# Optimization experiments

Measured on AMD Instinct MI355X. Metric: run time of the kernel, lower is better.

Reference implementation:

```python
import jax, jax.numpy as jnp
import numpy as np

N_NODES = 100000
N_EDGES = 3200000
N_GRAPHS = 512
F_IN = 35
F_OUT = 128


def setup_inputs() -> dict:
    key = jax.random.key(0)
    ks = jax.random.split(key, 16)
    x = jax.random.normal(ks[0], (N_NODES, F_IN), dtype=jnp.float32)
    edge_index = jax.random.randint(ks[1], (2, N_EDGES), 0, N_NODES, dtype=jnp.int32)
    batch = jnp.sort(jax.random.randint(ks[2], (N_NODES,), 0, N_GRAPHS, dtype=jnp.int32))
    def lin(k, fin, fout):
        s = 1.0 / np.sqrt(fin)
        return jax.random.uniform(k, (fin, fout), jnp.float32, -s, s)
    return {
        "x": x, "edge_index": edge_index, "batch": batch,
        # SAGEConv 1 (35 -> 35): lin_l acts on aggregated neighbors (has bias), lin_r on root (no bias)
        "Wl1": lin(ks[3], F_IN, F_IN), "bl1": jnp.zeros((F_IN,), jnp.float32), "Wr1": lin(ks[4], F_IN, F_IN),
        # SAGEConv 2 (35 -> 128)
        "Wl2": lin(ks[5], F_IN, F_OUT), "bl2": jnp.zeros((F_OUT,), jnp.float32), "Wr2": lin(ks[6], F_IN, F_OUT),
        # FC head
        "Wg1": lin(ks[7], F_OUT, F_OUT), "bg1": jnp.zeros((F_OUT,), jnp.float32),
        "Wg2": lin(ks[8], F_OUT, F_OUT), "bg2": jnp.zeros((F_OUT,), jnp.float32),
        "Wo": lin(ks[9], F_OUT, 1), "bo": jnp.zeros((1,), jnp.float32),
    }


def _sage_conv(x, src, dst, Wl, bl, Wr):
    # mean aggregation over incoming edges (src -> dst), PyG SAGEConv default
    msg = x[src]                                               # [E, F] gather
    s = jax.ops.segment_sum(msg, dst, num_segments=N_NODES)    # [N, F]
    cnt = jax.ops.segment_sum(jnp.ones((src.shape[0],), x.dtype), dst, num_segments=N_NODES)
    agg = s / jnp.maximum(cnt, 1.0)[:, None]
    return agg @ Wl + bl + x @ Wr


def reference(x, edge_index, batch, Wl1, bl1, Wr1, Wl2, bl2, Wr2, Wg1, bg1, Wg2, bg2, Wo, bo):
    src, dst = edge_index[0], edge_index[1]
    h = _sage_conv(x, src, dst, Wl1, bl1, Wr1)   # [N, 35]
    h = jax.nn.relu(h)
    h = _sage_conv(h, src, dst, Wl2, bl2, Wr2)   # [N, 128]
    # global max pool over each graph in the batch
    g = jax.ops.segment_max(h, batch, num_segments=N_GRAPHS)  # [G, 128]
    g = jax.nn.relu(g @ Wg1 + bg1)
    g = jax.nn.relu(g @ Wg2 + bg2)
    return g @ Wo + bo                            # [G, 1]
```

## Files before the change

kernel.cpp:

```cpp
#include <hip/hip_runtime.h>
#include <hip/hip_bf16.h>
#include <math.h>

#define FIN 35
#define FOUT 128
#define NGRAPHS 512
#define PWA 32
#define PWB 4
#define RP 36
#define STRIP1 64
#define STRIP2 32
#define CHUNK 8192
#define MAXBUCK 512
#define MAXBE 12288

typedef _Float16 half8 __attribute__((ext_vector_type(8)));
typedef _Float16 half4 __attribute__((ext_vector_type(4)));

__device__ __forceinline__ unsigned int enc_f32(float f) {
    unsigned int u = __float_as_uint(f);
    return (u & 0x80000000u) ? ~u : (u | 0x80000000u);
}
__device__ __forceinline__ float dec_f32(unsigned int u) {
    unsigned int b = (u & 0x80000000u) ? (u ^ 0x80000000u) : ~u;
    return __uint_as_float(b);
}


__global__ __launch_bounds__(256) void hist1_kernel(const int* __restrict__ dst,
                                                    int* __restrict__ counts,
                                                    int E, int nblk1, int nbuck) {
    __shared__ int h[MAXBUCK];
    for (int t = threadIdx.x; t < nbuck; t += 256) h[t] = 0;
    __syncthreads();
    int base = blockIdx.x * CHUNK;
    int end = min(base + CHUNK, E);
    for (int e = base + threadIdx.x; e < end; e += 256)
        atomicAdd(&h[dst[e] >> 8], 1);
    __syncthreads();
    for (int t = threadIdx.x; t < nbuck; t += 256)
        counts[t * nblk1 + blockIdx.x] = h[t];
}

__global__ void partial_reduce_kernel(const int* __restrict__ v_in, int* __restrict__ partial, int SC) {
    int i = blockIdx.x * 256 + threadIdx.x;
    int v = (i < SC) ? v_in[i] : 0;
    #pragma unroll
    for (int off = 32; off > 0; off >>= 1) v += __shfl_down(v, off, 64);
    __shared__ int w[4];
    if ((threadIdx.x & 63) == 0) w[threadIdx.x >> 6] = v;
    __syncthreads();
    if (threadIdx.x == 0) partial[blockIdx.x] = w[0] + w[1] + w[2] + w[3];
}

__global__ void scan_partials_kernel(int* __restrict__ partial, int NB) {
    __shared__ int lds[1024];
    int t = threadIdx.x;
    int v = (t < NB) ? partial[t] : 0;
    lds[t] = v;
    __syncthreads();
    for (int off = 1; off < 1024; off <<= 1) {
        int tv = (t >= off) ? lds[t - off] : 0;
        __syncthreads();
        lds[t] += tv;
        __syncthreads();
    }
    if (t < NB) partial[t] = lds[t] - v;
}

__global__ void scan_final_kernel(const int* __restrict__ v_in, const int* __restrict__ partial,
                                  int* __restrict__ outx, int SC) {
    __shared__ int lds[256];
    int i = blockIdx.x * 256 + threadIdx.x;
    int v = (i < SC) ? v_in[i] : 0;
    lds[threadIdx.x] = v;
    __syncthreads();
    for (int off = 1; off < 256; off <<= 1) {
        int tv = (threadIdx.x >= off) ? lds[threadIdx.x - off] : 0;
        __syncthreads();
        lds[threadIdx.x] += tv;
        __syncthreads();
    }
    int excl = lds[threadIdx.x] - v + partial[blockIdx.x];
    if (i < SC) {
        outx[i] = excl;
        if (i == SC - 1) outx[SC] = excl + v;
    }
}

__global__ __launch_bounds__(256) void scatter1_kernel(const int* __restrict__ src,
                                                       const int* __restrict__ dst,
                                                       const int* __restrict__ offs,
                                                       int* __restrict__ ebuf,
                                                       int E, int nblk1, int nbuck) {
    __shared__ int cur[MAXBUCK];
    for (int t = threadIdx.x; t < nbuck; t += 256) cur[t] = offs[t * nblk1 + blockIdx.x];
    __syncthreads();
    int base = blockIdx.x * CHUNK;
    int end = min(base + CHUNK, E);
    for (int e = base + threadIdx.x; e < end; e += 256) {
        int d = dst[e];
        int p = atomicAdd(&cur[d >> 8], 1);
        ebuf[p] = (src[e] << 8) | (d & 255);
    }
}

__global__ __launch_bounds__(256) void csr2_kernel(const int* __restrict__ ebuf,
                                                   const int* __restrict__ offs,
                                                   int* __restrict__ row_ptr,
                                                   int* __restrict__ hsplit,
                                                   int* __restrict__ esrc,
                                                   int E, int nblk1, int nbuck, int N, int halfN) {
    __shared__ int h[512];
    __shared__ int scn[256];
    __shared__ int cur[512];
    __shared__ int e_sh[MAXBE];
    int b = blockIdx.x;
    int t = threadIdx.x;
    int bstart = offs[b * nblk1];
    int bend = (b + 1 < nbuck) ? offs[(b + 1) * nblk1] : E;
    int cnt = bend - bstart;
    bool fit = (cnt <= MAXBE);

    if (fit)
        for (int k = t; k < cnt; k += 256) e_sh[k] = ebuf[bstart + k];
    h[t] = 0; h[t + 256] = 0;
    __syncthreads();
    for (int k = t; k < cnt; k += 256) {
        int e = fit ? e_sh[k] : ebuf[bstart + k];
        int bin = ((e & 255) << 1) | ((e >> 8) >= halfN ? 1 : 0);
        atomicAdd(&h[bin], 1);
    }
    __syncthreads();

    int v0 = h[2 * t];
    int v1 = h[2 * t + 1];
    int pair = v0 + v1;
    scn[t] = pair;
    __syncthreads();
    for (int off = 1; off < 256; off <<= 1) {
        int tv = (t >= off) ? scn[t - off] : 0;
        __syncthreads();
        scn[t] += tv;
        __syncthreads();
    }
    int base = bstart + scn[t] - pair;
    int node = (b << 8) + t;
    if (node < N) {
        row_ptr[node] = base;
        hsplit[node] = base + v0;
    }
    if (b == 0 && t == 0) row_ptr[N] = E;
    cur[2 * t] = base;
    cur[2 * t + 1] = base + v0;
    __syncthreads();

    for (int k = t; k < cnt; k += 256) {
        int e = fit ? e_sh[k] : ebuf[bstart + k];
        int bin = ((e & 255) << 1) | ((e >> 8) >= halfN ? 1 : 0);
        int p = atomicAdd(&cur[bin], 1);
        esrc[p] = e >> 8;
    }
}

__global__ void repack_kernel(const float* __restrict__ x,
                              _Float16* __restrict__ xA, _Float16* __restrict__ xB, int N) {
    int t = blockIdx.x * 256 + threadIdx.x;
    int NA = N * PWA;
    if (t < NA) {
        int n = t >> 5;
        int f = t & 31;
        xA[t] = (_Float16)x[(long long)n * FIN + f];
    } else if (t < NA + N * PWB) {
        int c = t - NA;
        int n = c >> 2;
        int f3 = c & 3;
        float v = (f3 < 3) ? x[(long long)n * FIN + 32 + f3] : 0.0f;
        xB[c] = (_Float16)v;
    }
}

__global__ __launch_bounds__(256) void gather3_kernel(const _Float16* __restrict__ pA,
                                                      const _Float16* __restrict__ pB,
                                                      const int* __restrict__ row_ptr,
                                                      const int* __restrict__ hsplit,
                                                      const int* __restrict__ esrc,
                                                      float* __restrict__ spA,
                                                      float* __restrict__ spB,
                                                      int N, int Wtot, int WS) {
    int q = blockIdx.x & 7;
    int m = blockIdx.x >> 3;
    int w = q * WS + m * 256 + threadIdx.x;
    int wend = min((q + 1) * WS, Wtot);
    if (w >= wend) return;
    int NI = N * 8;
    int pass = w / NI;
    int t = w - pass * NI;
    int n = t >> 3;

    if (pass < 2) {
        int quad = (t >> 1) & 3;
        int q2 = t & 1;
        int b = (pass == 0) ? row_ptr[n] : hsplit[n];
        int e = (pass == 0) ? hsplit[n] : row_ptr[n + 1];
        int len = e - b;
        int k0 = b + ((len * q2) >> 1);
        int k1 = b + ((len * (q2 + 1)) >> 1);
        const _Float16* base = pA + (quad << 3);

        float a0[8] = {0,0,0,0,0,0,0,0}, a1[8] = {0,0,0,0,0,0,0,0};
        float a2[8] = {0,0,0,0,0,0,0,0}, a3[8] = {0,0,0,0,0,0,0,0};
        int k = k0;
        for (; k + 4 <= k1; k += 4) {
            int s0 = esrc[k], s1 = esrc[k + 1], s2 = esrc[k + 2], s3 = esrc[k + 3];
            half8 v0 = *(const half8*)(base + ((long long)s0 << 5));
            half8 v1 = *(const half8*)(base + ((long long)s1 << 5));
            half8 v2 = *(const half8*)(base + ((long long)s2 << 5));
            half8 v3 = *(const half8*)(base + ((long long)s3 << 5));
            #pragma unroll
            for (int i = 0; i < 8; ++i) {
                a0[i] += (float)v0[i];
                a1[i] += (float)v1[i];
                a2[i] += (float)v2[i];
                a3[i] += (float)v3[i];
            }
        }
        for (; k < k1; ++k) {
            half8 v = *(const half8*)(base + ((long long)esrc[k] << 5));
            #pragma unroll
            for (int i = 0; i < 8; ++i) a0[i] += (float)v[i];
        }

        float s[8];
        #pragma unroll
        for (int i = 0; i < 8; ++i) {
            float p = (a0[i] + a1[i]) + (a2[i] + a3[i]);
            p += __shfl_xor(p, 1, 64);
            s[i] = p;
        }
        if (q2 == 0) {
            float* outp = spA + ((long long)pass * N + n) * PWA + (quad << 3);
            float4 r0, r1;
            r0.x = s[0]; r0.y = s[1]; r0.z = s[2]; r0.w = s[3];
            r1.x = s[4]; r1.y = s[5]; r1.z = s[6]; r1.w = s[7];
            *(float4*)outp = r0;
            *(float4*)(outp + 4) = r1;
        }
    } else {
        int q8 = t & 7;
        int b = row_ptr[n];
        int e = row_ptr[n + 1];
        int len = e - b;
        int k0 = b + ((len * q8) >> 3);
        int k1 = b + ((len * (q8 + 1)) >> 3);

        float a0[4] = {0,0,0,0}, a1[4] = {0,0,0,0};
        int k = k0;
        for (; k + 2 <= k1; k += 2) {
            int s0 = esrc[k], s1 = esrc[k + 1];
            half4 v0 = *(const half4*)(pB + ((long long)s0 << 2));
            half4 v1 = *(const half4*)(pB + ((long long)s1 << 2));
            #pragma unroll
            for (int i = 0; i < 4; ++i) {
                a0[i] += (float)v0[i];
                a1[i] += (float)v1[i];
            }
        }
        for (; k < k1; ++k) {
            half4 v = *(const half4*)(pB + ((long long)esrc[k] << 2));
            #pragma unroll
            for (int i = 0; i < 4; ++i) a0[i] += (float)v[i];
        }

        float s[4];
        #pragma unroll
        for (int i = 0; i < 4; ++i) {
            float p = a0[i] + a1[i];
            p += __shfl_xor(p, 1, 64);
            p += __shfl_xor(p, 2, 64);
            p += __shfl_xor(p, 4, 64);
            s[i] = p;
        }
        if (q8 == 0) {
            float4 r;
            r.x = s[0]; r.y = s[1]; r.z = s[2]; r.w = s[3];
            *(float4*)(spB + ((long long)n << 2)) = r;
        }
    }
}

__global__ __launch_bounds__(256) void nu1_kernel(const float* __restrict__ x,
                                                  const float* __restrict__ spA,
                                                  const float* __restrict__ spB,
                                                  const int* __restrict__ row_ptr,
                                                  const float* __restrict__ Wl,
                                                  const float* __restrict__ bl,
                                                  const float* __restrict__ Wr,
                                                  _Float16* __restrict__ h1A,
                                                  _Float16* __restrict__ h1B,
                                                  int N) {
    __shared__ float x_sh[STRIP1 * RP];
    __shared__ float s_sh[STRIP1 * RP];
    __shared__ int deg_sh[STRIP1];

    int node0 = blockIdx.x * STRIP1;
    if (node0 >= N) return;
    int nn = min(STRIP1, N - node0);
    int tot = nn * FIN;

    for (int t = threadIdx.x; t < STRIP1; t += 256) {
        x_sh[t * RP + 35] = 0.0f;
        s_sh[t * RP + 35] = 0.0f;
    }
    if (threadIdx.x < nn)
        deg_sh[threadIdx.x] = row_ptr[node0 + threadIdx.x + 1] - row_ptr[node0 + threadIdx.x];
    for (int t = threadIdx.x; t < tot; t += 256) {
        int nl = t / FIN;
        int i = t - nl * FIN;
        long long node = node0 + nl;
        x_sh[nl * RP + i] = x[node * FIN + i];
        float sv = (i < 32) ? (spA[node * PWA + i] + spA[((long long)N + node) * PWA + i])
                            : spB[(node << 2) + (i - 32)];
        s_sh[nl * RP + i] = sv;
    }
    __syncthreads();

    int wave = threadIdx.x >> 6;
    int j = threadIdx.x & 63;
    if (j >= FIN) return;

    float wl[36], wr[36];
    #pragma unroll
    for (int i = 0; i < FIN; ++i) {
        wl[i] = Wl[i * FIN + j];
        wr[i] = Wr[i * FIN + j];
    }
    wl[35] = 0.0f; wr[35] = 0.0f;
    float blj = bl[j];

    int nstart = wave * 16;
    int nend = min(nstart + 16, nn);
    for (int nl = nstart; nl < nend; ++nl) {
        float accS = 0.0f;
        float accX = blj;
        #pragma unroll
        for (int c = 0; c < 9; ++c) {
            float4 sv = *(const float4*)&s_sh[nl * RP + 4 * c];
            float4 xv = *(const float4*)&x_sh[nl * RP + 4 * c];
            accS = fmaf(sv.x, wl[4 * c],     accS);
            accS = fmaf(sv.y, wl[4 * c + 1], accS);
            accS = fmaf(sv.z, wl[4 * c + 2], accS);
            accS = fmaf(sv.w, wl[4 * c + 3], accS);
            accX = fmaf(xv.x, wr[4 * c],     accX);
            accX = fmaf(xv.y, wr[4 * c + 1], accX);
            accX = fmaf(xv.z, wr[4 * c + 2], accX);
            accX = fmaf(xv.w, wr[4 * c + 3], accX);
        }
        float inv = 1.0f / (float)max(deg_sh[nl], 1);
        float acc = fmaxf(fmaf(accS, inv, accX), 0.0f);
        long long node = node0 + nl;
        if (j < 32) {
            h1A[(node << 5) + j] = (_Float16)acc;
        } else {
            h1B[(node << 2) + (j - 32)] = (_Float16)acc;
            if (j == 34) h1B[(node << 2) + 3] = (_Float16)0.0f;
        }
    }
}

__global__ __launch_bounds__(128) void nu2_pool_kernel(const _Float16* __restrict__ h1A,
                                                       const _Float16* __restrict__ h1B,
                                                       const float* __restrict__ spA,
                                                       const float* __restrict__ spB,
                                                       const int* __restrict__ row_ptr,
                                                       const float* __restrict__ Wl,
                                                       const float* __restrict__ bl,
                                                       const float* __restrict__ Wr,
                                                       const int* __restrict__ batch,
                                                       unsigned int* __restrict__ genc,
                                                       int N) {
    __shared__ float s_sh[STRIP2 * RP];
    __shared__ float h_sh[STRIP2 * RP];
    __shared__ int b_sh[STRIP2];
    __shared__ int deg_sh[STRIP2];
    int node0 = blockIdx.x * STRIP2;
    if (node0 >= N) return;
    int nn = min(STRIP2, N - node0);
    int tot = nn * FIN;

    for (int t = threadIdx.x; t < STRIP2; t += 128) {
        s_sh[t * RP + 35] = 0.0f;
        h_sh[t * RP + 35] = 0.0f;
    }
    if (threadIdx.x < nn) {
        b_sh[threadIdx.x] = batch[node0 + threadIdx.x];
        deg_sh[threadIdx.x] = row_ptr[node0 + threadIdx.x + 1] - row_ptr[node0 + threadIdx.x];
    }
    for (int t = threadIdx.x; t < tot; t += 128) {
        int nl = t / FIN;
        int i = t - nl * FIN;
        long long node = node0 + nl;
        float hv = (i < 32) ? (float)h1A[(node << 5) + i]
                            : (float)h1B[(node << 2) + (i - 32)];
        h_sh[nl * RP + i] = hv;
        float sv = (i < 32) ? (spA[node * PWA + i] + spA[((long long)N + node) * PWA + i])
                            : spB[(node << 2) + (i - 32)];
        s_sh[nl * RP + i] = sv;
    }
    __syncthreads();

    int j = threadIdx.x;
    float wl[36], wr[36];
    #pragma unroll
    for (int i = 0; i < FIN; ++i) {
        wl[i] = Wl[i * FOUT + j];
        wr[i] = Wr[i * FOUT + j];
    }
    wl[35] = 0.0f; wr[35] = 0.0f;
    float blj = bl[j];

    int curg = b_sh[0];
    float m = -INFINITY;
    for (int nl = 0; nl < nn; ++nl) {
        float accS = 0.0f;
        float accH = blj;
        #pragma unroll
        for (int c = 0; c < 9; ++c) {
            float4 sv = *(const float4*)&s_sh[nl * RP + 4 * c];
            float4 hv = *(const float4*)&h_sh[nl * RP + 4 * c];
            accS = fmaf(sv.x, wl[4 * c],     accS);
            accS = fmaf(sv.y, wl[4 * c + 1], accS);
            accS = fmaf(sv.z, wl[4 * c + 2], accS);
            accS = fmaf(sv.w, wl[4 * c + 3], accS);
            accH = fmaf(hv.x, wr[4 * c],     accH);
            accH = fmaf(hv.y, wr[4 * c + 1], accH);
            accH = fmaf(hv.z, wr[4 * c + 2], accH);
            accH = fmaf(hv.w, wr[4 * c + 3], accH);
        }
        float inv = 1.0f / (float)max(deg_sh[nl], 1);
        float acc = fmaf(accS, inv, accH);
        int g = b_sh[nl];
        if (g != curg) {
            atomicMax(&genc[curg * FOUT + j], enc_f32(m));
            curg = g;
            m = acc;
        } else {
            m = fmaxf(m, acc);
        }
    }
    atomicMax(&genc[curg * FOUT + j], enc_f32(m));
}

__global__ void head_kernel(const unsigned int* __restrict__ genc,
                            const float* __restrict__ Wg1, const float* __restrict__ bg1,
                            const float* __restrict__ Wg2, const float* __restrict__ bg2,
                            const float* __restrict__ Wo,  const float* __restrict__ bo,
                            float* __restrict__ out) {
    __shared__ float a[FOUT];
    __shared__ float c[FOUT];
    __shared__ float red[2];
    int g = blockIdx.x;
    int j = threadIdx.x;

    a[j] = dec_f32(genc[g * FOUT + j]);
    __syncthreads();

    float acc = bg1[j];
    #pragma unroll 8
    for (int i = 0; i < FOUT; ++i) acc = fmaf(a[i], Wg1[i * FOUT + j], acc);
    c[j] = fmaxf(acc, 0.0f);
    __syncthreads();

    acc = bg2[j];
    #pragma unroll 8
    for (int i = 0; i < FOUT; ++i) acc = fmaf(c[i], Wg2[i * FOUT + j], acc);
    float t = fmaxf(acc, 0.0f) * Wo[j];

    #pragma unroll
    for (int off = 32; off > 0; off >>= 1) t += __shfl_down(t, off, 64);
    if ((threadIdx.x & 63) == 0) red[threadIdx.x >> 6] = t;
    __syncthreads();
    if (threadIdx.x == 0) out[g] = red[0] + red[1] + bo[0];
}

extern "C" void kernel_launch(void* const* d_in, const int* in_sizes, int n_in,
                              void* d_out, int out_size, void* d_ws, size_t ws_size,
                              hipStream_t stream) {
    const float* x    = (const float*)d_in[0];
    const int*   ei   = (const int*)  d_in[1];
    const int*   batch= (const int*)  d_in[2];
    const float* Wl1  = (const float*)d_in[3];
    const float* bl1  = (const float*)d_in[4];
    const float* Wr1  = (const float*)d_in[5];
    const float* Wl2  = (const float*)d_in[6];
    const float* bl2  = (const float*)d_in[7];
    const float* Wr2  = (const float*)d_in[8];
    const float* Wg1  = (const float*)d_in[9];
    const float* bg1  = (const float*)d_in[10];
    const float* Wg2  = (const float*)d_in[11];
    const float* bg2  = (const float*)d_in[12];
    const float* Wo   = (const float*)d_in[13];
    const float* bo   = (const float*)d_in[14];
    float* out = (float*)d_out;

    const int N = in_sizes[0] / FIN;
    const int E = in_sizes[1] / 2;
    const int* src = ei;
    const int* dst = ei + E;
    const int halfN = N >> 1;

    const int nblk1 = (E + CHUNK - 1) / CHUNK;
    const int nbuck = (N + 255) >> 8;
    const int SC = nbuck * nblk1;
    const int NB2 = (SC + 255) / 256;

    char* ws = (char*)d_ws;
    size_t off = 0;
    auto alloc = [&](size_t bytes) { char* p = ws + off; off += (bytes + 255) & ~255ull; return p; };
    int*          counts  = (int*)alloc((size_t)SC * 4);
    int*          offs    = (int*)alloc((size_t)(SC + 1) * 4);
    int*          partial = (int*)alloc(1024 * 4);
    int*          row_ptr = (int*)alloc((size_t)(N + 1) * 4);
    int*          hsplit  = (int*)alloc((size_t)N * 4);
    int*          esrc    = (int*)alloc((size_t)E * 4);
    char*         regionA = (char*)alloc((size_t)E * 4);
    _Float16*     xA      = (_Float16*)alloc((size_t)N * PWA * 2);
    _Float16*     xB      = (_Float16*)alloc((size_t)N * PWB * 2);
    float*        spA     = (float*)alloc((size_t)2 * N * PWA * 4);
    float*        spB     = (float*)alloc((size_t)N * PWB * 4);
    unsigned int* genc    = (unsigned int*)alloc((size_t)NGRAPHS * FOUT * 4);
    int*       ebuf = (int*)regionA;
    _Float16*  h1A  = (_Float16*)regionA;
    _Float16*  h1B  = (_Float16*)(regionA + (size_t)N * PWA * 2);
    (void)ws_size; (void)n_in; (void)out_size;

    const int BS = 256;
    const int Wtot = N * 24;
    int WS = ((Wtot / 8 + BS - 1) / BS) * BS;
    const int bpx = WS / BS;
    const int rpb = (N * 36 + BS - 1) / BS;
    int nu1b = (N + STRIP1 - 1) / STRIP1;
    int nu2b = (N + STRIP2 - 1) / STRIP2;

    hipLaunchKernelGGL(hist1_kernel, dim3(nblk1), dim3(BS), 0, stream, dst, counts, E, nblk1, nbuck);
    hipLaunchKernelGGL(partial_reduce_kernel, dim3(NB2), dim3(BS), 0, stream, counts, partial, SC);
    hipLaunchKernelGGL(scan_partials_kernel, dim3(1), dim3(1024), 0, stream, partial, NB2);
    hipLaunchKernelGGL(scan_final_kernel, dim3(NB2), dim3(BS), 0, stream, counts, partial, offs, SC);
    hipLaunchKernelGGL(scatter1_kernel, dim3(nblk1), dim3(BS), 0, stream, src, dst, offs, ebuf, E, nblk1, nbuck);
    hipLaunchKernelGGL(csr2_kernel, dim3(nbuck), dim3(BS), 0, stream,
                       ebuf, offs, row_ptr, hsplit, esrc, E, nblk1, nbuck, N, halfN);

    hipLaunchKernelGGL(repack_kernel, dim3(rpb), dim3(BS), 0, stream, x, xA, xB, N);
    hipLaunchKernelGGL(gather3_kernel, dim3(8 * bpx), dim3(BS), 0, stream,
                       xA, xB, row_ptr, hsplit, esrc, spA, spB, N, Wtot, WS);
    hipLaunchKernelGGL(nu1_kernel, dim3(nu1b), dim3(BS), 0, stream,
                       x, spA, spB, row_ptr, Wl1, bl1, Wr1, h1A, h1B, N);

    hipLaunchKernelGGL(gather3_kernel, dim3(8 * bpx), dim3(BS), 0, stream,
                       h1A, h1B, row_ptr, hsplit, esrc, spA, spB, N, Wtot, WS);
    hipMemsetAsync(genc, 0, (size_t)NGRAPHS * FOUT * 4, stream);
    hipLaunchKernelGGL(nu2_pool_kernel, dim3(nu2b), dim3(128), 0, stream,
                       h1A, h1B, spA, spB, row_ptr, Wl2, bl2, Wr2, batch, genc, N);

    hipLaunchKernelGGL(head_kernel, dim3(NGRAPHS), dim3(FOUT), 0, stream,
                       genc, Wg1, bg1, Wg2, bg2, Wo, bo, out);
}
```

Before: 371.2 us.

## Use MFMA fp16 matrix cores for second SAGE layer with split-weight precision

Replaces the scalar FMA per-node loop of the second SAGEConv plus max-pool with a 64-node-strip kernel that packs the mean-aggregated neighbours and root features into a swizzled fp16 LDS tile and multiplies them with a concatenated [Wl;Wr] matrix using 16x16x32 f16 MFMA. A small prep kernel splits the weights into high and low fp16 parts, so two MFMA passes recover near-fp32 weight precision, and writes them in fragment layout. The activations are rounded to fp16, which adds precision risk. The pooling then reads the results back from LDS and does atomicMax per graph run.

```diff
diff --git a/kernel.cpp b/kernel.cpp
--- a/kernel.cpp
+++ b/kernel.cpp
@@ -9,13 +9,17 @@
 #define PWB 4
 #define RP 36
 #define STRIP1 64
-#define STRIP2 32
 #define CHUNK 8192
 #define MAXBUCK 512
 #define MAXBE 12288
 
+#define STRIPM 64
+#define HROW 130
+#define NFRAG 48
+
 typedef _Float16 half8 __attribute__((ext_vector_type(8)));
 typedef _Float16 half4 __attribute__((ext_vector_type(4)));
+typedef float f32x4 __attribute__((ext_vector_type(4)));
 
 __device__ __forceinline__ unsigned int enc_f32(float f) {
     unsigned int u = __float_as_uint(f);
@@ -368,87 +372,207 @@
     }
 }
 
-__global__ __launch_bounds__(128) void nu2_pool_kernel(const _Float16* __restrict__ h1A,
-                                                       const _Float16* __restrict__ h1B,
-                                                       const float* __restrict__ spA,
-                                                       const float* __restrict__ spB,
-                                                       const int* __restrict__ row_ptr,
-                                                       const float* __restrict__ Wl,
-                                                       const float* __restrict__ bl,
-                                                       const float* __restrict__ Wr,
-                                                       const int* __restrict__ batch,
-                                                       unsigned int* __restrict__ genc,
-                                                       int N) {
-    __shared__ float s_sh[STRIP2 * RP];
-    __shared__ float h_sh[STRIP2 * RP];
-    __shared__ int b_sh[STRIP2];
-    __shared__ int deg_sh[STRIP2];
-    int node0 = blockIdx.x * STRIP2;
+__global__ void wprep2_kernel(const float* __restrict__ Wl, const float* __restrict__ Wr,
+                              _Float16* __restrict__ wfrag) {
+    int f = blockIdx.x;
+    int l = threadIdx.x;
+    int ps = f / 24;
+    int rem = f % 24;
+    int ks = rem >> 3;
+    int nt = rem & 7;
+    int n = nt * 16 + (l & 15);
+    int kb = ks * 32 + ((l >> 4) << 3);
+    half8 o;
+    #pragma unroll
+    for (int e = 0; e < 8; ++e) {
+        int k = kb + e;
+        float v = 0.0f;
+        if (k < 35) v = Wl[k * FOUT + n];
+        else if (k >= 36 && k < 71) v = Wr[(k - 36) * FOUT + n];
+        _Float16 hi = (_Float16)v;
+        o[e] = ps ? (_Float16)(v - (float)hi) : hi;
+    }
+    *(half8*)(wfrag + ((size_t)f * 64 + l) * 8) = o;
+}
+
+__global__ __launch_bounds__(256) void nu2_pool_mfma_kernel(const _Float16* __restrict__ h1A,
+                                                            const _Float16* __restrict__ h1B,
+                                                            const float* __restrict__ spA,
+                                                            const float* __restrict__ spB,
+                                                            const int* __restrict__ row_ptr,
+                                                            const _Float16* __restrict__ wfrag,
+                                                            const float* __restrict__ bl,
+                                                            const int* __restrict__ batch,
+                                                            unsigned int* __restrict__ genc,
+                                                            int N) {
+    __shared__ __align__(16) float h_sh[STRIPM * HROW];
+    __shared__ int b_sh[STRIPM];
+
+    int node0 = blockIdx.x * STRIPM;
     if (node0 >= N) return;
-    int nn = min(STRIP2, N - node0);
-    int tot = nn * FIN;
-
-    for (int t = threadIdx.x; t < STRIP2; t += 128) {
-        s_sh[t * RP + 35] = 0.0f;
-        h_sh[t * RP + 35] = 0.0f;
-    }
-    if (threadIdx.x < nn) {
-        b_sh[threadIdx.x] = batch[node0 + threadIdx.x];
-        deg_sh[threadIdx.x] = row_ptr[node0 + threadIdx.x + 1] - row_ptr[node0 + threadIdx.x];
-    }
-    for (int t = threadIdx.x; t < tot; t += 128) {
-        int nl = t / FIN;
-        int i = t - nl * FIN;
-        long long node = node0 + nl;
-        float hv = (i < 32) ? (float)h1A[(node << 5) + i]
-                            : (float)h1B[(node << 2) + (i - 32)];
-        h_sh[nl * RP + i] = hv;
-        float sv = (i < 32) ? (spA[node * PWA + i] + spA[((long long)N + node) * PWA + i])
-                            : spB[(node << 2) + (i - 32)];
-        s_sh[nl * RP + i] = sv;
-    }
-    __syncthreads();
-
-    int j = threadIdx.x;
-    float wl[36], wr[36];
+    int nn = min(STRIPM, N - node0);
+
+    char* Ab = (char*)h_sh;
+    const int t = threadIdx.x;
+    const int lane = t & 63;
+    const int wv = t >> 6;
+
+    {
+        const int r = lane;
+        const long long node = (long long)node0 + r;
+        const bool valid = (r < nn);
+        const int sw = r & 7;
+        char* rowp = Ab + r * 256;
+
+        if (wv == 0) {
+            int dg = 1;
+            if (valid) dg = row_ptr[node + 1] - row_ptr[node];
+            float inv = 1.0f / (float)max(dg, 1);
+            #pragma unroll
+            for (int u = 0; u < 3; ++u) {
+                half8 h = {0,0,0,0,0,0,0,0};
+                if (valid) {
+                    const float* p = spA + node * 32 + u * 8;
+                    const float* q = spA + ((long long)N + node) * 32 + u * 8;
+                    float4 p0 = *(const float4*)p;
+                    float4 p1 = *(const float4*)(p + 4);
+                    float4 q0 = *(const float4*)q;
+                    float4 q1 = *(const float4*)(q + 4);
+                    h[0] = (_Float16)((p0.x + q0.x) * inv);
+                    h[1] = (_Float16)((p0.y + q0.y) * inv);
+                    h[2] = (_Float16)((p0.z + q0.z) * inv);
+                    h[3] = (_Float16)((p0.w + q0.w) * inv);
+                    h[4] = (_Float16)((p1.x + q1.x) * inv);
+                    h[5] = (_Float16)((p1.y + q1.y) * inv);
+                    h[6] = (_Float16)((p1.z + q1.z) * inv);
+                    h[7] = (_Float16)((p1.w + q1.w) * inv);
+                }
+                *(half8*)(rowp + ((u ^ sw) << 4)) = h;
+            }
+        } else if (wv == 1) {
+            int dg = 1;
+            if (valid) dg = row_ptr[node + 1] - row_ptr[node];
+            float inv = 1.0f / (float)max(dg, 1);
+            half8 h3 = {0,0,0,0,0,0,0,0};
+            half8 h4 = {0,0,0,0,0,0,0,0};
+            half8 h5 = {0,0,0,0,0,0,0,0};
+            if (valid) {
+                const float* p = spA + node * 32 + 24;
+                const float* q = spA + ((long long)N + node) * 32 + 24;
+                float4 p0 = *(const float4*)p;
+                float4 p1 = *(const float4*)(p + 4);
+                float4 q0 = *(const float4*)q;
+                float4 q1 = *(const float4*)(q + 4);
+                h3[0] = (_Float16)((p0.x + q0.x) * inv);
+                h3[1] = (_Float16)((p0.y + q0.y) * inv);
+                h3[2] = (_Float16)((p0.z + q0.z) * inv);
+                h3[3] = (_Float16)((p0.w + q0.w) * inv);
+                h3[4] = (_Float16)((p1.x + q1.x) * inv);
+                h3[5] = (_Float16)((p1.y + q1.y) * inv);
+                h3[6] = (_Float16)((p1.z + q1.z) * inv);
+                h3[7] = (_Float16)((p1.w + q1.w) * inv);
+                float4 sb = *(const float4*)(spB + (node << 2));
+                half4 ha = *(const half4*)(h1A + (node << 5));
+                h4[0] = (_Float16)(sb.x * inv);
+                h4[1] = (_Float16)(sb.y * inv);
+                h4[2] = (_Float16)(sb.z * inv);
+                h4[3] = (_Float16)(sb.w * inv);
+                h4[4] = ha[0]; h4[5] = ha[1]; h4[6] = ha[2]; h4[7] = ha[3];
+                half4 hb0 = *(const half4*)(h1A + (node << 5) + 4);
+                half4 hb1 = *(const half4*)(h1A + (node << 5) + 8);
+                h5[0] = hb0[0]; h5[1] = hb0[1]; h5[2] = hb0[2]; h5[3] = hb0[3];
+                h5[4] = hb1[0]; h5[5] = hb1[1]; h5[6] = hb1[2]; h5[7] = hb1[3];
+            }
+            *(half8*)(rowp + ((3 ^ sw) << 4)) = h3;
+            *(half8*)(rowp + ((4 ^ sw) << 4)) = h4;
+            *(half8*)(rowp + ((5 ^ sw) << 4)) = h5;
+        } else if (wv == 2) {
+            half8 h6 = {0,0,0,0,0,0,0,0};
+            half8 h7 = {0,0,0,0,0,0,0,0};
+            half8 h8 = {0,0,0,0,0,0,0,0};
+            if (valid) {
+                half4 a0 = *(const half4*)(h1A + (node << 5) + 12);
+                half4 a1 = *(const half4*)(h1A + (node << 5) + 16);
+                half4 a2 = *(const half4*)(h1A + (node << 5) + 20);
+                half4 a3 = *(const half4*)(h1A + (node << 5) + 24);
+                half4 a4 = *(const half4*)(h1A + (node << 5) + 28);
+                half4 b4 = *(const half4*)(h1B + (node << 2));
+                h6[0] = a0[0]; h6[1] = a0[1]; h6[2] = a0[2]; h6[3] = a0[3];
+                h6[4] = a1[0]; h6[5] = a1[1]; h6[6] = a1[2]; h6[7] = a1[3];
+                h7[0] = a2[0]; h7[1] = a2[1]; h7[2] = a2[2]; h7[3] = a2[3];
+                h7[4] = a3[0]; h7[5] = a3[1]; h7[6] = a3[2]; h7[7] = a3[3];
+                h8[0] = a4[0]; h8[1] = a4[1]; h8[2] = a4[2]; h8[3] = a4[3];
+                h8[4] = b4[0]; h8[5] = b4[1]; h8[6] = b4[2]; h8[7] = b4[3];
+            }
+            *(half8*)(rowp + ((6 ^ sw) << 4)) = h6;
+            *(half8*)(rowp + ((7 ^ sw) << 4)) = h7;
+            *(half8*)(rowp + ((8 ^ sw) << 4)) = h8;
+        } else {
+            half8 z = {0,0,0,0,0,0,0,0};
+            *(half8*)(rowp + ((9  ^ sw) << 4)) = z;
+            *(half8*)(rowp + ((10 ^ sw) << 4)) = z;
+            *(half8*)(rowp + ((11 ^ sw) << 4)) = z;
+            if (lane < nn) b_sh[lane] = batch[node0 + lane];
+        }
+    }
+    __syncthreads();
+
+    f32x4 acc[8];
     #pragma unroll
-    for (int i = 0; i < FIN; ++i) {
-        wl[i] = Wl[i * FOUT + j];
-        wr[i] = Wr[i * FOUT + j];
-    }
-    wl[35] = 0.0f; wr[35] = 0.0f;
-    float blj = bl[j];
-
-    int curg = b_sh[0];
-    float m = -INFINITY;
-    for (int nl = 0; nl < nn; ++nl) {
-        float accS = 0.0f;
-        float accH = blj;
+    for (int nt = 0; nt < 8; ++nt) acc[nt] = (f32x4){0.0f, 0.0f, 0.0f, 0.0f};
+
+    const int m0 = wv << 4;
+    const int rr = m0 + (lane & 15);
+    const int rsw = lane & 7;
+    const int g = lane >> 4;
+    const char* arow = Ab + rr * 256;
+
+    #pragma unroll
+    for (int ps = 0; ps < 2; ++ps) {
         #pragma unroll
-        for (int c = 0; c < 9; ++c) {
-            float4 sv = *(const float4*)&s_sh[nl * RP + 4 * c];
-            float4 hv = *(const float4*)&h_sh[nl * RP + 4 * c];
-            accS = fmaf(sv.x, wl[4 * c],     accS);
-            accS = fmaf(sv.y, wl[4 * c + 1], accS);
-            accS = fmaf(sv.z, wl[4 * c + 2], accS);
-            accS = fmaf(sv.w, wl[4 * c + 3], accS);
-            accH = fmaf(hv.x, wr[4 * c],     accH);
-            accH = fmaf(hv.y, wr[4 * c + 1], accH);
-            accH = fmaf(hv.z, wr[4 * c + 2], accH);
-            accH = fmaf(hv.w, wr[4 * c + 3], accH);
-        }
-        float inv = 1.0f / (float)max(deg_sh[nl], 1);
-        float acc = fmaf(accS, inv, accH);
-        int g = b_sh[nl];
-        if (g != curg) {
-            atomicMax(&genc[curg * FOUT + j], enc_f32(m));
-            curg = g;
-            m = acc;
-        } else {
-            m = fmaxf(m, acc);
-        }
-    }
-    atomicMax(&genc[curg * FOUT + j], enc_f32(m));
+        for (int ks = 0; ks < 3; ++ks) {
+            half8 af = *(const half8*)(arow + ((((ks << 2) + g) ^ rsw) << 4));
+            const _Float16* wp = wfrag + ((size_t)((ps * 3 + ks) << 3) * 64 + lane) * 8;
+            #pragma unroll
+            for (int nt = 0; nt < 8; ++nt) {
+                half8 bf = *(const half8*)(wp + (size_t)nt * 512);
+                acc[nt] = __builtin_amdgcn_mfma_f32_16x16x32_f16(af, bf, acc[nt], 0, 0, 0);
+            }
+        }
+    }
+    __syncthreads();
+
+    const int col = lane & 15;
+    const int rbase = m0 + (g << 2);
+    #pragma unroll
+    for (int nt = 0; nt < 8; ++nt) {
+        float bb = bl[(nt << 4) + col];
+        #pragma unroll
+        for (int q2 = 0; q2 < 4; ++q2)
+            h_sh[(rbase + q2) * HROW + (nt << 4) + col] = acc[nt][q2] + bb;
+    }
+    __syncthreads();
+
+    const int j = t & 127;
+    const int hh = t >> 7;
+    int nl = hh << 5;
+    int nend = min(nl + 32, nn);
+    if (nl < nend) {
+        int curg = b_sh[nl];
+        float mx = -INFINITY;
+        for (; nl < nend; ++nl) {
+            float v = h_sh[nl * HROW + j];
+            int gb = b_sh[nl];
+            if (gb != curg) {
+                atomicMax(&genc[curg * FOUT + j], enc_f32(mx));
+                curg = gb;
+                mx = v;
+            } else {
+                mx = fmaxf(mx, v);
+            }
+        }
+        atomicMax(&genc[curg * FOUT + j], enc_f32(mx));
+    }
 }
 
 __global__ void head_kernel(const unsigned int* __restrict__ genc,
@@ -529,9 +653,10 @@
     float*        spA     = (float*)alloc((size_t)2 * N * PWA * 4);
     float*        spB     = (float*)alloc((size_t)N * PWB * 4);
     unsigned int* genc    = (unsigned int*)alloc((size_t)NGRAPHS * FOUT * 4);
-    int*       ebuf = (int*)regionA;
-    _Float16*  h1A  = (_Float16*)regionA;
-    _Float16*  h1B  = (_Float16*)(regionA + (size_t)N * PWA * 2);
+    int*       ebuf  = (int*)regionA;
+    _Float16*  h1A   = (_Float16*)regionA;
+    _Float16*  h1B   = (_Float16*)(regionA + (size_t)N * PWA * 2);
+    _Float16*  wfrag = (_Float16*)(regionA + (size_t)N * (PWA + PWB) * 2);
     (void)ws_size; (void)n_in; (void)out_size;
 
     const int BS = 256;
@@ -540,7 +665,7 @@
     const int bpx = WS / BS;
     const int rpb = (N * 36 + BS - 1) / BS;
     int nu1b = (N + STRIP1 - 1) / STRIP1;
-    int nu2b = (N + STRIP2 - 1) / STRIP2;
+    int nu2b = (N + STRIPM - 1) / STRIPM;
 
     hipLaunchKernelGGL(hist1_kernel, dim3(nblk1), dim3(BS), 0, stream, dst, counts, E, nblk1, nbuck);
     hipLaunchKernelGGL(partial_reduce_kernel, dim3(NB2), dim3(BS), 0, stream, counts, partial, SC);
@@ -550,6 +675,8 @@
     hipLaunchKernelGGL(csr2_kernel, dim3(nbuck), dim3(BS), 0, stream,
                        ebuf, offs, row_ptr, hsplit, esrc, E, nblk1, nbuck, N, halfN);
 
+    hipLaunchKernelGGL(wprep2_kernel, dim3(NFRAG), dim3(64), 0, stream, Wl2, Wr2, wfrag);
+
     hipLaunchKernelGGL(repack_kernel, dim3(rpb), dim3(BS), 0, stream, x, xA, xB, N);
     hipLaunchKernelGGL(gather3_kernel, dim3(8 * bpx), dim3(BS), 0, stream,
                        xA, xB, row_ptr, hsplit, esrc, spA, spB, N, Wtot, WS);
@@ -559,8 +686,8 @@
     hipLaunchKernelGGL(gather3_kernel, dim3(8 * bpx), dim3(BS), 0, stream,
                        h1A, h1B, row_ptr, hsplit, esrc, spA, spB, N, Wtot, WS);
     hipMemsetAsync(genc, 0, (size_t)NGRAPHS * FOUT * 4, stream);
-    hipLaunchKernelGGL(nu2_pool_kernel, dim3(nu2b), dim3(128), 0, stream,
-                       h1A, h1B, spA, spB, row_ptr, Wl2, bl2, Wr2, batch, genc, N);
+    hipLaunchKernelGGL(nu2_pool_mfma_kernel, dim3(nu2b), dim3(BS), 0, stream,
+                       h1A, h1B, spA, spB, row_ptr, wfrag, bl2, batch, genc, N);
 
     hipLaunchKernelGGL(head_kernel, dim3(NGRAPHS), dim3(FOUT), 0, stream,
                        genc, Wg1, bg1, Wg2, bg2, Wo, bo, out);
```

Result: faster. 341.4 us (-8.0%).
